# Optimization experiments

Hardware: AMD Instinct MI355X
Metric: run time of the kernel (lower is better)

Reference implementation:

```python
import jax, jax.numpy as jnp
import numpy as np

B, N, L, D, IN, H = 16, 100, 90, 300, 256, 256


def setup_inputs() -> dict:
    key = jax.random.key(0)
    ks = jax.random.split(key, 24)
    s = 0.02
    inp = {}
    inp["h_local"] = jax.random.normal(ks[0], (B, N, IN), jnp.float32)
    inp["items_review"] = jax.random.normal(ks[1], (B, N, L, D), jnp.float32)
    inp["adj_sg"] = jax.random.randint(ks[2], (B, N, 2 * N), 0, 2, jnp.int32)
    inp["attn_review_mask"] = jnp.zeros((B, N, L), jnp.bool_)
    # BatchNorm affine params (eval mode, running_mean=0, running_var=1)
    inp["bn_gamma"] = jnp.ones((IN,), jnp.float32)
    inp["bn_beta"] = jnp.zeros((IN,), jnp.float32)
    # MultiHeadAttention linear layers (review_dim=300)
    inp["W_q"] = jax.random.normal(ks[3], (D, D), jnp.float32) * s
    inp["b_q"] = jnp.zeros((D,), jnp.float32)
    inp["W_k"] = jax.random.normal(ks[4], (D, D), jnp.float32) * s
    inp["b_k"] = jnp.zeros((D,), jnp.float32)
    inp["W_v"] = jax.random.normal(ks[5], (D, D), jnp.float32) * s
    inp["b_v"] = jnp.zeros((D,), jnp.float32)
    inp["W_f"] = jax.random.normal(ks[6], (D, D), jnp.float32) * s
    inp["b_f"] = jnp.zeros((D,), jnp.float32)
    # fc: input_size -> hidden_size
    inp["W_fc"] = jax.random.normal(ks[7], (H, IN), jnp.float32) * s
    inp["b_fc"] = jnp.zeros((H,), jnp.float32)
    # edge linear layers
    inp["W_in"] = jax.random.normal(ks[8], (H, H), jnp.float32) * s
    inp["b_in"] = jnp.zeros((H,), jnp.float32)
    inp["W_out"] = jax.random.normal(ks[9], (H, H), jnp.float32) * s
    inp["b_out"] = jnp.zeros((H,), jnp.float32)
    inp["b_iah"] = jax.random.normal(ks[10], (H,), jnp.float32) * s
    inp["b_oah"] = jax.random.normal(ks[11], (H,), jnp.float32) * s
    # fc_in_out: 2H -> H
    inp["W_io"] = jax.random.normal(ks[12], (H, 2 * H), jnp.float32) * s
    inp["b_io"] = jnp.zeros((H,), jnp.float32)
    return inp


def reference(h_local, items_review, adj_sg, attn_review_mask,
              bn_gamma, bn_beta,
              W_q, b_q, W_k, b_k, W_v, b_v, W_f, b_f,
              W_fc, b_fc, W_in, b_in, W_out, b_out,
              b_iah, b_oah, W_io, b_io):
    n = h_local.shape[1]
    # BatchNorm1d (eval mode: running_mean=0, running_var=1) + fc
    h = h_local * (bn_gamma / jnp.sqrt(1.0 + 1e-5)) + bn_beta
    hidden = h @ W_fc.T + b_fc                                  # [B,N,H]

    # MultiHeadAttention over reviews (heads never split in original bmm)
    q = items_review @ W_q.T + b_q                              # [B,N,L,D]
    k = items_review @ W_k.T + b_k
    v = items_review @ W_v.T + b_v
    scale = (items_review.shape[-1] // 3) ** (-0.5)             # (300//3)^-0.5 = 0.1
    attn = jax.nn.softmax(jnp.einsum('bnld,bnmd->bnlm', q, k) * scale, axis=-1)
    ctx = jnp.einsum('bnlm,bnmd->bnld', attn, v)
    out_attn = items_review + (ctx @ W_f.T + b_f)               # residual
    h_review = jnp.sum(out_attn, axis=2)                        # [B,N,D] sum over review_len

    # pairwise cosine similarity (torch.cosine_similarity, eps=1e-8)
    norms = jnp.linalg.norm(h_review, axis=-1)                  # [B,N]
    sim = jnp.einsum('bnd,bmd->bnm', h_review, h_review) \
        / jnp.maximum(norms[:, :, None] * norms[:, None, :], 1e-8)

    adj_in = adj_sg[:, :, :n] > 0
    adj_out = adj_sg[:, :, n:2 * n] > 0
    NEG = jnp.float32(-9e15)
    sim_in = jax.nn.softmax(jnp.where(adj_in, sim, NEG), axis=-1)
    sim_out = jax.nn.softmax(jnp.where(adj_out, sim, NEG), axis=-1)

    input_in = jnp.einsum('bnm,bmh->bnh', sim_in, hidden @ W_in.T + b_in) + b_iah
    input_out = jnp.einsum('bnm,bmh->bnh', sim_out, hidden @ W_out.T + b_out) + b_oah
    output = jnp.concatenate([input_in, input_out], axis=-1) @ W_io.T + b_io
    return output
```

## Files before the change

### kernel.cpp

```cpp
#include <hip/hip_runtime.h>
#include <math.h>

#define Bb 16
#define Nn 100
#define Ll 90
#define Dd 300
#define NBLK (Bb*Nn)
#define LP 96
#define DP 320
#define DPH 40

typedef __attribute__((ext_vector_type(8))) short short8v;
typedef __attribute__((ext_vector_type(4))) short short4v;
typedef __attribute__((ext_vector_type(4))) float f32x4;

__device__ __forceinline__ unsigned short f2bf(float f) {
  unsigned int u = __float_as_uint(f);
  u += 0x7fffu + ((u >> 16) & 1u);
  return (unsigned short)(u >> 16);
}
__device__ __forceinline__ float bf2f(unsigned short h) {
  return __uint_as_float(((unsigned int)h) << 16);
}

__global__ __launch_bounds__(256) void k_matM(const float* __restrict__ Wq,
                                              const float* __restrict__ Wk,
                                              unsigned short* __restrict__ Mb) {
  int idx = blockIdx.x * 256 + threadIdx.x;
  if (idx >= DP * DP) return;
  int i = idx / DP, j = idx % DP;
  float s = 0.f;
  if (i < Dd && j < Dd) {
    for (int o = 0; o < Dd; o++) s += Wq[o * Dd + i] * Wk[o * Dd + j];
  }
  Mb[idx] = f2bf(s);
}

__global__ __launch_bounds__(256) void k_matG(const float* __restrict__ Wf,
                                              const float* __restrict__ Wv,
                                              float* __restrict__ G) {
  int idx = blockIdx.x * 256 + threadIdx.x;
  if (idx >= Dd * 304) return;
  int o = idx / 304, p = idx % 304;
  float s = 0.f;
  if (p < Dd) {
    for (int v = 0; v < Dd; v++) s += Wf[o * Dd + v] * Wv[v * Dd + p];
  }
  G[idx] = s;
}

__global__ void k_vec(const float* __restrict__ Wq, const float* __restrict__ Wk,
                      const float* __restrict__ Wf,
                      const float* __restrict__ bq, const float* __restrict__ bk,
                      const float* __restrict__ bv, const float* __restrict__ bf,
                      float* __restrict__ uv, float* __restrict__ tv,
                      float* __restrict__ cv, float* __restrict__ bias2) {
  int t = threadIdx.x;
  if (t < 304) {
    float su = 0.f, st = 0.f, sb = 0.f;
    if (t < Dd) {
      for (int o = 0; o < Dd; o++) {
        su += Wq[o * Dd + t] * bk[o];
        st += Wk[o * Dd + t] * bq[o];
      }
      for (int v = 0; v < Dd; v++) sb += Wf[t * Dd + v] * bv[v];
      sb = 90.f * (sb + bf[t]);
    }
    uv[t] = su; tv[t] = st; bias2[t] = sb;
  }
  if (t == 511) {
    float s = 0.f;
    for (int o = 0; o < Dd; o++) s += bq[o] * bk[o];
    cv[0] = s;
  }
}

__global__ __launch_bounds__(256) void k_mm256(
    const float* __restrict__ A0, const float* __restrict__ A1, int lda,
    const float* __restrict__ B0, const float* __restrict__ B1, int ldb,
    float* __restrict__ C, int ldc, const float* __restrict__ gamma) {
  const float* A = blockIdx.z ? A1 : A0;
  const float* B = blockIdx.z ? B1 : B0;
  float* Cb = C + (size_t)blockIdx.z * 256 * ldc;
  __shared__ float As[16][68];
  __shared__ float Bs[16][68];
  int m0 = blockIdx.x * 64, n0 = blockIdx.y * 64;
  int tx = threadIdx.x & 15, ty = threadIdx.x >> 4;
  float acc[4][4];
#pragma unroll
  for (int i = 0; i < 4; i++)
#pragma unroll
    for (int j = 0; j < 4; j++) acc[i][j] = 0.f;
  int r = threadIdx.x >> 2;
  int kq = (threadIdx.x & 3) << 2;
  int kk2 = threadIdx.x >> 4;
  int nq = (threadIdx.x & 15) << 2;
  for (int k0 = 0; k0 < 256; k0 += 16) {
    {
      float4 v = *(const float4*)(A + (size_t)(m0 + r) * lda + k0 + kq);
      As[kq + 0][r] = v.x; As[kq + 1][r] = v.y; As[kq + 2][r] = v.z; As[kq + 3][r] = v.w;
    }
    {
      float4 v = *(const float4*)(B + (size_t)(k0 + kk2) * ldb + n0 + nq);
      Bs[kk2][nq + 0] = v.x; Bs[kk2][nq + 1] = v.y; Bs[kk2][nq + 2] = v.z; Bs[kk2][nq + 3] = v.w;
    }
    __syncthreads();
#pragma unroll
    for (int kk = 0; kk < 16; kk++) {
      float4 av = *(const float4*)&As[kk][ty * 4];
      float4 bv = *(const float4*)&Bs[kk][tx * 4];
      acc[0][0] += av.x * bv.x; acc[0][1] += av.x * bv.y; acc[0][2] += av.x * bv.z; acc[0][3] += av.x * bv.w;
      acc[1][0] += av.y * bv.x; acc[1][1] += av.y * bv.y; acc[1][2] += av.y * bv.z; acc[1][3] += av.y * bv.w;
      acc[2][0] += av.z * bv.x; acc[2][1] += av.z * bv.y; acc[2][2] += av.z * bv.z; acc[2][3] += av.z * bv.w;
      acc[3][0] += av.w * bv.x; acc[3][1] += av.w * bv.y; acc[3][2] += av.w * bv.z; acc[3][3] += av.w * bv.w;
    }
    __syncthreads();
  }
  const float bninv = rsqrtf(1.00001f);
#pragma unroll
  for (int i = 0; i < 4; i++) {
    int gm = m0 + ty * 4 + i;
#pragma unroll
    for (int j = 0; j < 4; j++) {
      int gn = n0 + tx * 4 + j;
      float v = acc[i][j];
      if (gamma) v *= gamma[gn] * bninv;
      Cb[(size_t)gm * ldc + gn] = v;
    }
  }
}

__global__ __launch_bounds__(256) void k_vecd(
    const float* __restrict__ W_fc, const float* __restrict__ b_fc,
    const float* __restrict__ beta,
    const float* __restrict__ W_in, const float* __restrict__ b_in,
    const float* __restrict__ b_iah,
    const float* __restrict__ W_out, const float* __restrict__ b_out,
    const float* __restrict__ b_oah,
    const float* __restrict__ W_io, const float* __restrict__ b_io,
    float* __restrict__ dvec) {
  __shared__ float v1[256];
  __shared__ float v23[512];
  int i = threadIdx.x;
  float s = 0.f;
  for (int k = 0; k < 256; k++) s += W_fc[i * 256 + k] * beta[k];
  v1[i] = s + b_fc[i];
  __syncthreads();
  float s2 = 0.f, s3 = 0.f;
  for (int k = 0; k < 256; k++) {
    float vk = v1[k];
    s2 += W_in[i * 256 + k] * vk;
    s3 += W_out[i * 256 + k] * vk;
  }
  v23[i] = s2 + b_in[i] + b_iah[i];
  v23[256 + i] = s3 + b_out[i] + b_oah[i];
  __syncthreads();
  float sd = 0.f;
  for (int k = 0; k < 512; k++) sd += W_io[i * 512 + k] * v23[k];
  dvec[i] = sd + b_io[i];
}

__global__ __launch_bounds__(512, 4) void k_attn(
    const float* __restrict__ items, const unsigned short* __restrict__ Mb,
    const float* __restrict__ uvec, const float* __restrict__ tvec,
    const float* __restrict__ cval_p,
    float* __restrict__ r_all, float* __restrict__ colsum_all) {
  __shared__ unsigned short Xs[LP * DP];
  __shared__ unsigned short Zc[LP * 64];
  __shared__ float ulv[LP], tmv[LP], wsum[LP];
  __shared__ float ulds[304], tlds[304];

  const int tid = threadIdx.x;
  const int bid = blockIdx.x;
  const float* Xg = items + (size_t)bid * (Ll * Dd);
  const float cval = cval_p[0];

  for (int c = tid; c < LP * DPH; c += 512) {
    int l = c / DPH, ch = c % DPH, d0 = ch * 8;
    float v[8];
    if (l < Ll && d0 < Dd) {
      if (d0 + 8 <= Dd) {
        float4 a = *(const float4*)(Xg + l * Dd + d0);
        float4 b = *(const float4*)(Xg + l * Dd + d0 + 4);
        v[0] = a.x; v[1] = a.y; v[2] = a.z; v[3] = a.w;
        v[4] = b.x; v[5] = b.y; v[6] = b.z; v[7] = b.w;
      } else {
#pragma unroll
        for (int q = 0; q < 8; q++) { int d = d0 + q; v[q] = (d < Dd) ? Xg[l * Dd + d] : 0.f; }
      }
    } else {
#pragma unroll
      for (int q = 0; q < 8; q++) v[q] = 0.f;
    }
    short8v pk;
#pragma unroll
    for (int q = 0; q < 8; q++) pk[q] = (short)f2bf(v[q]);
    *(short8v*)((char*)Xs + l * 640 + ((d0 * 2) ^ ((l & 7) << 4))) = pk;
  }
  for (int d = tid; d < 304; d += 512) { ulds[d] = uvec[d]; tlds[d] = tvec[d]; }
  if (tid < LP) wsum[tid] = 0.f;
  for (int d = tid; d < 304; d += 512) {
    float s = 0.f;
    if (d < Dd) {
      for (int l = 0; l < Ll; l++) s += Xg[l * Dd + d];
    }
    colsum_all[(size_t)bid * 304 + d] = s;
  }
  __syncthreads();

  if (tid < 384) {
    int row = tid >> 2, q = tid & 3;
    float su = 0.f, st = 0.f;
    if (row < Ll) {
      for (int ii = 0; ii < 75; ii++) {
        int i = q * 75 + ii;
        float xv = bf2f(Xs[(row * 640 + ((i * 2) ^ ((row & 7) << 4))) >> 1]);
        su += xv * ulds[i];
        st += xv * tlds[i];
      }
    }
    su += __shfl_xor(su, 1); su += __shfl_xor(su, 2);
    st += __shfl_xor(st, 1); st += __shfl_xor(st, 2);
    if (q == 0) { ulv[row] = su; tmv[row] = st; }
  }
  __syncthreads();

  const int lane = tid & 63, wave = tid >> 6;
  const int fr = lane & 15, kg = lane >> 4;

  f32x4 acc[6];
#pragma unroll
  for (int mt = 0; mt < 6; mt++) acc[mt] = (f32x4){0.f, 0.f, 0.f, 0.f};

  for (int c = 0; c < 5; c++) {
    for (int t = wave; t < 24; t += 8) {
      int ict = t / 6, mt = t % 6;
      int irow = c * 64 + ict * 16 + fr;
      f32x4 zacc = (f32x4){0.f, 0.f, 0.f, 0.f};
#pragma unroll
      for (int ks = 0; ks < 10; ks++) {
        short8v a = *(const short8v*)(Mb + irow * DP + ks * 32 + kg * 8);
        int brow = mt * 16 + fr;
        short8v b = *(const short8v*)((char*)Xs + brow * 640 +
                                      (((ks * 32 + kg * 8) * 2) ^ ((brow & 7) << 4)));
        zacc = __builtin_amdgcn_mfma_f32_16x16x32_bf16(a, b, zacc, 0, 0, 0);
      }
      int m = mt * 16 + fr;
      int ic0 = ict * 16 + kg * 4;
      short4v pk;
#pragma unroll
      for (int r2 = 0; r2 < 4; r2++) pk[r2] = (short)f2bf(zacc[r2]);
      *(short4v*)((char*)Zc + m * 128 + ((ic0 * 2) ^ ((m & 7) << 4))) = pk;
    }
    __syncthreads();
    if (wave < 6) {
#pragma unroll
      for (int mt = 0; mt < 6; mt++) {
#pragma unroll
        for (int ks = 0; ks < 2; ks++) {
          int arow = wave * 16 + fr;
          short8v a = *(const short8v*)((char*)Xs + arow * 640 +
                                        (((c * 64 + ks * 32 + kg * 8) * 2) ^ ((arow & 7) << 4)));
          int brow = mt * 16 + fr;
          short8v b = *(const short8v*)((char*)Zc + brow * 128 +
                                        (((ks * 32 + kg * 8) * 2) ^ ((brow & 7) << 4)));
          acc[mt] = __builtin_amdgcn_mfma_f32_16x16x32_bf16(a, b, acc[mt], 0, 0, 0);
        }
      }
    }
    __syncthreads();
  }

  if (wave < 6) {
    float tmc[6];
#pragma unroll
    for (int mt = 0; mt < 6; mt++) tmc[mt] = tmv[mt * 16 + fr];
    float colpart[6] = {0.f, 0.f, 0.f, 0.f, 0.f, 0.f};
#pragma unroll
    for (int r2 = 0; r2 < 4; r2++) {
      int l = wave * 16 + kg * 4 + r2;
      float base = ulv[l] + cval;
      float x[6];
#pragma unroll
      for (int mt = 0; mt < 6; mt++) {
        int col = mt * 16 + fr;
        x[mt] = (col < Ll) ? 0.1f * (acc[mt][r2] + base + tmc[mt]) : -INFINITY;
      }
      float mx = x[0];
#pragma unroll
      for (int mt = 1; mt < 6; mt++) mx = fmaxf(mx, x[mt]);
      mx = fmaxf(mx, __shfl_xor(mx, 1));
      mx = fmaxf(mx, __shfl_xor(mx, 2));
      mx = fmaxf(mx, __shfl_xor(mx, 4));
      mx = fmaxf(mx, __shfl_xor(mx, 8));
      float e[6]; float s = 0.f;
#pragma unroll
      for (int mt = 0; mt < 6; mt++) { e[mt] = __expf(x[mt] - mx); s += e[mt]; }
      s += __shfl_xor(s, 1); s += __shfl_xor(s, 2);
      s += __shfl_xor(s, 4); s += __shfl_xor(s, 8);
      float inv = 1.f / s;
      if (l < Ll) {
#pragma unroll
        for (int mt = 0; mt < 6; mt++) colpart[mt] += e[mt] * inv;
      }
    }
#pragma unroll
    for (int mt = 0; mt < 6; mt++) {
      colpart[mt] += __shfl_xor(colpart[mt], 16);
      colpart[mt] += __shfl_xor(colpart[mt], 32);
    }
    if (lane < 16) {
#pragma unroll
      for (int mt = 0; mt < 6; mt++) atomicAdd(&wsum[mt * 16 + fr], colpart[mt]);
    }
  }
  __syncthreads();

  for (int i = tid; i < 304; i += 512) {
    float s = 0.f;
    if (i < Dd) {
      for (int m = 0; m < Ll; m++)
        s += wsum[m] * bf2f(Xs[(m * 640 + ((i * 2) ^ ((m & 7) << 4))) >> 1]);
    }
    r_all[(size_t)bid * 304 + i] = s;
  }
}

__global__ __launch_bounds__(256) void k_gemm_bt(
    const float* __restrict__ A, int lda, const float* __restrict__ W, int ldw,
    const float* __restrict__ bias, const float* __restrict__ res, int ldres,
    float* __restrict__ C, int ldc, int Mdim, int Ndim, int Kdim) {
  __shared__ float As[16][68];
  __shared__ float Bs[16][68];
  int m0 = blockIdx.x * 64, n0 = blockIdx.y * 64;
  int tx = threadIdx.x & 15, ty = threadIdx.x >> 4;
  float acc[4][4];
#pragma unroll
  for (int i = 0; i < 4; i++)
#pragma unroll
    for (int j = 0; j < 4; j++) acc[i][j] = 0.f;
  int r = threadIdx.x >> 2;
  int kq = (threadIdx.x & 3) << 2;
  for (int k0 = 0; k0 < Kdim; k0 += 16) {
    {
      int gm = m0 + r;
      float4 v = {0.f, 0.f, 0.f, 0.f};
      if (gm < Mdim) v = *(const float4*)(A + (size_t)gm * lda + k0 + kq);
      As[kq + 0][r] = v.x; As[kq + 1][r] = v.y; As[kq + 2][r] = v.z; As[kq + 3][r] = v.w;
    }
    {
      int gn = n0 + r;
      float4 v = {0.f, 0.f, 0.f, 0.f};
      if (gn < Ndim) v = *(const float4*)(W + (size_t)gn * ldw + k0 + kq);
      Bs[kq + 0][r] = v.x; Bs[kq + 1][r] = v.y; Bs[kq + 2][r] = v.z; Bs[kq + 3][r] = v.w;
    }
    __syncthreads();
#pragma unroll
    for (int kk = 0; kk < 16; kk++) {
      float4 av = *(const float4*)&As[kk][ty * 4];
      float4 bv = *(const float4*)&Bs[kk][tx * 4];
      acc[0][0] += av.x * bv.x; acc[0][1] += av.x * bv.y; acc[0][2] += av.x * bv.z; acc[0][3] += av.x * bv.w;
      acc[1][0] += av.y * bv.x; acc[1][1] += av.y * bv.y; acc[1][2] += av.y * bv.z; acc[1][3] += av.y * bv.w;
      acc[2][0] += av.z * bv.x; acc[2][1] += av.z * bv.y; acc[2][2] += av.z * bv.z; acc[2][3] += av.z * bv.w;
      acc[3][0] += av.w * bv.x; acc[3][1] += av.w * bv.y; acc[3][2] += av.w * bv.z; acc[3][3] += av.w * bv.w;
    }
    __syncthreads();
  }
#pragma unroll
  for (int i = 0; i < 4; i++) {
    int gm = m0 + ty * 4 + i;
    if (gm >= Mdim) continue;
#pragma unroll
    for (int j = 0; j < 4; j++) {
      int gn = n0 + tx * 4 + j;
      if (gn >= Ndim) continue;
      float v = acc[i][j];
      if (bias) v += bias[gn];
      if (res) v += res[(size_t)gm * ldres + gn];
      C[(size_t)gm * ldc + gn] = v;
    }
  }
}

__global__ __launch_bounds__(256) void k_norm(const float* __restrict__ hrev,
                                              unsigned short* __restrict__ Hn) {
  int row = blockIdx.x * 4 + (threadIdx.x >> 6);
  int lane = threadIdx.x & 63;
  float v[5]; float ss = 0.f;
#pragma unroll
  for (int j = 0; j < 5; j++) {
    int i = lane + j * 64;
    float x = (i < Dd) ? hrev[(size_t)row * 304 + i] : 0.f;
    v[j] = x; ss += x * x;
  }
#pragma unroll
  for (int o = 32; o; o >>= 1) ss += __shfl_xor(ss, o);
  float inv = (ss > 0.f) ? rsqrtf(ss) : 0.f;
#pragma unroll
  for (int j = 0; j < 5; j++) {
    int i = lane + j * 64;
    if (i < DP) Hn[(size_t)row * DP + i] = f2bf(v[j] * inv);
  }
}

__global__ __launch_bounds__(512) void k_simgram(
    const unsigned short* __restrict__ Hn, const int* __restrict__ adj,
    float* __restrict__ simin, float* __restrict__ simout) {
  __shared__ unsigned short HL[112 * DP];
  int b = blockIdx.x, tid = threadIdx.x;
  for (int c = tid; c < 112 * DPH; c += 512) {
    int rb = c / DPH, ch = c % DPH;
    short8v v;
    if (rb < Nn) v = *(const short8v*)(Hn + ((size_t)(b * Nn + rb)) * DP + ch * 8);
    else {
#pragma unroll
      for (int q = 0; q < 8; q++) v[q] = 0;
    }
    *(short8v*)((char*)HL + rb * 640 + ((ch * 16) ^ ((rb & 7) << 4))) = v;
  }
  __syncthreads();
  const int lane = tid & 63, wave = tid >> 6;
  const int fr = lane & 15, kg = lane >> 4;
  if (wave < 7) {
    f32x4 acc[7];
#pragma unroll
    for (int mt = 0; mt < 7; mt++) acc[mt] = (f32x4){0.f, 0.f, 0.f, 0.f};
#pragma unroll
    for (int mt = 0; mt < 7; mt++) {
#pragma unroll
      for (int ks = 0; ks < 10; ks++) {
        int ar = wave * 16 + fr;
        short8v a = *(const short8v*)((char*)HL + ar * 640 +
                                      (((ks * 32 + kg * 8) * 2) ^ ((ar & 7) << 4)));
        int br = mt * 16 + fr;
        short8v bb = *(const short8v*)((char*)HL + br * 640 +
                                       (((ks * 32 + kg * 8) * 2) ^ ((br & 7) << 4)));
        acc[mt] = __builtin_amdgcn_mfma_f32_16x16x32_bf16(a, bb, acc[mt], 0, 0, 0);
      }
    }
    const int* adjb = adj + (size_t)b * Nn * 2 * Nn;
#pragma unroll
    for (int which = 0; which < 2; which++) {
      float* dst = which ? simout : simin;
#pragma unroll
      for (int r2 = 0; r2 < 4; r2++) {
        int l = wave * 16 + kg * 4 + r2;
        bool lv = l < Nn;
        float x[7];
#pragma unroll
        for (int mt = 0; mt < 7; mt++) {
          int col = mt * 16 + fr;
          bool cvd = col < Nn;
          int am = (lv && cvd) ? adjb[l * (2 * Nn) + which * Nn + col] : 0;
          x[mt] = cvd ? ((am > 0) ? acc[mt][r2] : -9e15f) : -INFINITY;
        }
        float mx = x[0];
#pragma unroll
        for (int mt = 1; mt < 7; mt++) mx = fmaxf(mx, x[mt]);
        mx = fmaxf(mx, __shfl_xor(mx, 1));
        mx = fmaxf(mx, __shfl_xor(mx, 2));
        mx = fmaxf(mx, __shfl_xor(mx, 4));
        mx = fmaxf(mx, __shfl_xor(mx, 8));
        float e[7]; float s = 0.f;
#pragma unroll
        for (int mt = 0; mt < 7; mt++) { e[mt] = __expf(x[mt] - mx); s += e[mt]; }
        s += __shfl_xor(s, 1); s += __shfl_xor(s, 2);
        s += __shfl_xor(s, 4); s += __shfl_xor(s, 8);
        float inv = 1.f / s;
        if (lv) {
#pragma unroll
          for (int mt = 0; mt < 7; mt++) {
            int col = mt * 16 + fr;
            if (col < Nn) dst[((size_t)(b * Nn + l)) * Nn + col] = e[mt] * inv;
          }
        }
      }
    }
  }
}

__global__ __launch_bounds__(256) void k_mixout(
    const float* __restrict__ simin, const float* __restrict__ simout,
    const float* __restrict__ P, const float* __restrict__ dvec,
    float* __restrict__ out) {
  __shared__ float si[Nn], so[Nn];
  int bn = blockIdx.x, h = threadIdx.x, b = bn / Nn;
  if (h < Nn) {
    si[h] = simin[(size_t)bn * Nn + h];
    so[h] = simout[(size_t)bn * Nn + h];
  }
  __syncthreads();
  const float* Pb = P + (size_t)b * Nn * 512;
  float acc = dvec[h];
  for (int m = 0; m < Nn; m++)
    acc += si[m] * Pb[m * 512 + h] + so[m] * Pb[m * 512 + 256 + h];
  out[(size_t)bn * 256 + h] = acc;
}

extern "C" void kernel_launch(void* const* d_in, const int* in_sizes, int n_in,
                              void* d_out, int out_size, void* d_ws, size_t ws_size,
                              hipStream_t stream) {
  (void)in_sizes; (void)n_in; (void)out_size; (void)ws_size;
  const float* h_local = (const float*)d_in[0];
  const float* items   = (const float*)d_in[1];
  const int*   adj     = (const int*)d_in[2];
  const float* bn_g  = (const float*)d_in[4];
  const float* bn_b  = (const float*)d_in[5];
  const float* W_q = (const float*)d_in[6];   const float* b_q = (const float*)d_in[7];
  const float* W_k = (const float*)d_in[8];   const float* b_k = (const float*)d_in[9];
  const float* W_v = (const float*)d_in[10];  const float* b_v = (const float*)d_in[11];
  const float* W_f = (const float*)d_in[12];  const float* b_f = (const float*)d_in[13];
  const float* W_fc = (const float*)d_in[14]; const float* b_fc = (const float*)d_in[15];
  const float* W_in = (const float*)d_in[16]; const float* b_in = (const float*)d_in[17];
  const float* W_out = (const float*)d_in[18]; const float* b_out = (const float*)d_in[19];
  const float* b_iah = (const float*)d_in[20]; const float* b_oah = (const float*)d_in[21];
  const float* W_io = (const float*)d_in[22];  const float* b_io = (const float*)d_in[23];
  float* out = (float*)d_out;

  char* w = (char*)d_ws;
  auto alloc = [&](size_t bytes) { char* p = w; w += (bytes + 255) & ~(size_t)255; return p; };
  unsigned short* Mb = (unsigned short*)alloc((size_t)DP * DP * 2);
  float* G      = (float*)alloc((size_t)Dd * 304 * 4);
  float* uv     = (float*)alloc(304 * 4);
  float* tv     = (float*)alloc(304 * 4);
  float* cv     = (float*)alloc(256);
  float* bias2  = (float*)alloc(304 * 4);
  float* Tbuf   = (float*)alloc((size_t)512 * 256 * 4);
  float* Bcat   = (float*)alloc((size_t)512 * 256 * 4);
  float* dvec   = (float*)alloc(256 * 4);
  float* r_all  = (float*)alloc((size_t)NBLK * 304 * 4);
  float* colsum = (float*)alloc((size_t)NBLK * 304 * 4);
  float* hrev   = (float*)alloc((size_t)NBLK * 304 * 4);
  unsigned short* Hn = (unsigned short*)alloc((size_t)NBLK * DP * 2);
  float* simin  = (float*)alloc((size_t)NBLK * Nn * 4);
  float* simout = (float*)alloc((size_t)NBLK * Nn * 4);
  float* P      = (float*)alloc((size_t)NBLK * 512 * 4);

  k_matM<<<(DP * DP + 255) / 256, 256, 0, stream>>>(W_q, W_k, Mb);
  k_matG<<<(Dd * 304 + 255) / 256, 256, 0, stream>>>(W_f, W_v, G);
  k_vec<<<1, 512, 0, stream>>>(W_q, W_k, W_f, b_q, b_k, b_v, b_f, uv, tv, cv, bias2);
  {
    dim3 g(4, 4, 2);
    k_mm256<<<g, 256, 0, stream>>>(W_in, W_out, 256, W_fc, W_fc, 256, Tbuf, 256, nullptr);
    k_mm256<<<g, 256, 0, stream>>>(W_io, W_io + 256, 512, Tbuf, Tbuf + 256 * 256, 256,
                                   Bcat, 256, bn_g);
  }
  k_vecd<<<1, 256, 0, stream>>>(W_fc, b_fc, bn_b, W_in, b_in, b_iah,
                                W_out, b_out, b_oah, W_io, b_io, dvec);

  {
    dim3 g(25, 8);
    k_gemm_bt<<<g, 256, 0, stream>>>(h_local, 256, Bcat, 256, nullptr, nullptr, 0,
                                     P, 512, NBLK, 512, 256);
  }

  k_attn<<<NBLK, 512, 0, stream>>>(items, Mb, uv, tv, cv, r_all, colsum);
  {
    dim3 g(25, 5);
    k_gemm_bt<<<g, 256, 0, stream>>>(r_all, 304, G, 304, bias2, colsum, 304,
                                     hrev, 304, NBLK, 300, 304);
  }
  k_norm<<<NBLK / 4, 256, 0, stream>>>(hrev, Hn);
  k_simgram<<<Bb, 512, 0, stream>>>(Hn, adj, simin, simout);
  k_mixout<<<NBLK, 256, 0, stream>>>(simin, simout, P, dvec, out);
}
```

Before: 775.8 us.

## Fold Q/K biases into augmented bilinear matrix and merge setup kernels

Adds a ones column at index 300 of the bf16 item tile and an extra row/column of the M matrix holding the bq/bk terms, so the bias corrections come out of the MFMA directly. That removes the per-row u/t dot products, their shared buffers and the k_vec kernel. The three weight-precompute kernels become one k_setup launch. The attention inner loop is restructured to keep three independent MFMA accumulators per wave with precomputed addresses. k_simgram is split into 7 single-wave blocks per batch that read from global memory, and several loops get unroll pragmas. The bias terms now go through bf16 rounding inside the MFMA, which may shift accuracy slightly.

```diff
diff --git a/kernel.cpp b/kernel.cpp
--- a/kernel.cpp
+++ b/kernel.cpp
@@ -23,55 +23,48 @@
   return __uint_as_float(((unsigned int)h) << 16);
 }
 
-__global__ __launch_bounds__(256) void k_matM(const float* __restrict__ Wq,
-                                              const float* __restrict__ Wk,
-                                              unsigned short* __restrict__ Mb) {
-  int idx = blockIdx.x * 256 + threadIdx.x;
-  if (idx >= DP * DP) return;
-  int i = idx / DP, j = idx % DP;
-  float s = 0.f;
-  if (i < Dd && j < Dd) {
-    for (int o = 0; o < Dd; o++) s += Wq[o * Dd + i] * Wk[o * Dd + j];
-  }
-  Mb[idx] = f2bf(s);
-}
-
-__global__ __launch_bounds__(256) void k_matG(const float* __restrict__ Wf,
-                                              const float* __restrict__ Wv,
-                                              float* __restrict__ G) {
-  int idx = blockIdx.x * 256 + threadIdx.x;
-  if (idx >= Dd * 304) return;
-  int o = idx / 304, p = idx % 304;
-  float s = 0.f;
-  if (p < Dd) {
-    for (int v = 0; v < Dd; v++) s += Wf[o * Dd + v] * Wv[v * Dd + p];
-  }
-  G[idx] = s;
-}
-
-__global__ void k_vec(const float* __restrict__ Wq, const float* __restrict__ Wk,
-                      const float* __restrict__ Wf,
-                      const float* __restrict__ bq, const float* __restrict__ bk,
-                      const float* __restrict__ bv, const float* __restrict__ bf,
-                      float* __restrict__ uv, float* __restrict__ tv,
-                      float* __restrict__ cv, float* __restrict__ bias2) {
-  int t = threadIdx.x;
-  if (t < 304) {
-    float su = 0.f, st = 0.f, sb = 0.f;
-    if (t < Dd) {
+__global__ __launch_bounds__(256) void k_setup(
+    const float* __restrict__ Wq, const float* __restrict__ Wk,
+    const float* __restrict__ bq, const float* __restrict__ bk,
+    const float* __restrict__ Wf, const float* __restrict__ Wv,
+    const float* __restrict__ bv, const float* __restrict__ bf,
+    unsigned short* __restrict__ Mb, float* __restrict__ G,
+    float* __restrict__ bias2) {
+  int blk = blockIdx.x;
+  if (blk < 400) {
+    int idx = blk * 256 + threadIdx.x;
+    int i = idx / DP, j = idx % DP;
+    float s = 0.f;
+    if (i <= Dd && j <= Dd) {
+#pragma unroll 10
       for (int o = 0; o < Dd; o++) {
-        su += Wq[o * Dd + t] * bk[o];
-        st += Wk[o * Dd + t] * bq[o];
-      }
-      for (int v = 0; v < Dd; v++) sb += Wf[t * Dd + v] * bv[v];
-      sb = 90.f * (sb + bf[t]);
-    }
-    uv[t] = su; tv[t] = st; bias2[t] = sb;
-  }
-  if (t == 511) {
-    float s = 0.f;
-    for (int o = 0; o < Dd; o++) s += bq[o] * bk[o];
-    cv[0] = s;
+        float av = (i < Dd) ? Wq[o * Dd + i] : bq[o];
+        float bw = (j < Dd) ? Wk[o * Dd + j] : bk[o];
+        s += av * bw;
+      }
+    }
+    Mb[idx] = f2bf(s);
+  } else if (blk < 757) {
+    int idx = (blk - 400) * 256 + threadIdx.x;
+    if (idx < Dd * 304) {
+      int o = idx / 304, p = idx % 304;
+      float s = 0.f;
+      if (p < Dd) {
+#pragma unroll 10
+        for (int v = 0; v < Dd; v++) s += Wf[o * Dd + v] * Wv[v * Dd + p];
+      }
+      G[idx] = s;
+    }
+  } else {
+    for (int t = threadIdx.x; t < 304; t += 256) {
+      float sb = 0.f;
+      if (t < Dd) {
+#pragma unroll 10
+        for (int v = 0; v < Dd; v++) sb += Wf[t * Dd + v] * bv[v];
+        sb = 90.f * (sb + bf[t]);
+      }
+      bias2[t] = sb;
+    }
   }
 }
 
@@ -143,10 +136,12 @@
   __shared__ float v23[512];
   int i = threadIdx.x;
   float s = 0.f;
+#pragma unroll 16
   for (int k = 0; k < 256; k++) s += W_fc[i * 256 + k] * beta[k];
   v1[i] = s + b_fc[i];
   __syncthreads();
   float s2 = 0.f, s3 = 0.f;
+#pragma unroll 16
   for (int k = 0; k < 256; k++) {
     float vk = v1[k];
     s2 += W_in[i * 256 + k] * vk;
@@ -156,24 +151,23 @@
   v23[256 + i] = s3 + b_out[i] + b_oah[i];
   __syncthreads();
   float sd = 0.f;
+#pragma unroll 16
   for (int k = 0; k < 512; k++) sd += W_io[i * 512 + k] * v23[k];
   dvec[i] = sd + b_io[i];
 }
 
 __global__ __launch_bounds__(512, 4) void k_attn(
     const float* __restrict__ items, const unsigned short* __restrict__ Mb,
-    const float* __restrict__ uvec, const float* __restrict__ tvec,
-    const float* __restrict__ cval_p,
     float* __restrict__ r_all, float* __restrict__ colsum_all) {
   __shared__ unsigned short Xs[LP * DP];
   __shared__ unsigned short Zc[LP * 64];
-  __shared__ float ulv[LP], tmv[LP], wsum[LP];
-  __shared__ float ulds[304], tlds[304];
+  __shared__ float wsum[LP];
 
   const int tid = threadIdx.x;
   const int bid = blockIdx.x;
   const float* Xg = items + (size_t)bid * (Ll * Dd);
-  const float cval = cval_p[0];
+
+  if (tid < LP) wsum[tid] = 0.f;
 
   for (int c = tid; c < LP * DPH; c += 512) {
     int l = c / DPH, ch = c % DPH, d0 = ch * 8;
@@ -186,7 +180,10 @@
         v[4] = b.x; v[5] = b.y; v[6] = b.z; v[7] = b.w;
       } else {
 #pragma unroll
-        for (int q = 0; q < 8; q++) { int d = d0 + q; v[q] = (d < Dd) ? Xg[l * Dd + d] : 0.f; }
+        for (int q = 0; q < 8; q++) {
+          int d = d0 + q;
+          v[q] = (d < Dd) ? Xg[l * Dd + d] : ((d == Dd) ? 1.f : 0.f);
+        }
       }
     } else {
 #pragma unroll
@@ -197,71 +194,73 @@
     for (int q = 0; q < 8; q++) pk[q] = (short)f2bf(v[q]);
     *(short8v*)((char*)Xs + l * 640 + ((d0 * 2) ^ ((l & 7) << 4))) = pk;
   }
-  for (int d = tid; d < 304; d += 512) { ulds[d] = uvec[d]; tlds[d] = tvec[d]; }
-  if (tid < LP) wsum[tid] = 0.f;
+
   for (int d = tid; d < 304; d += 512) {
     float s = 0.f;
     if (d < Dd) {
+#pragma unroll 18
       for (int l = 0; l < Ll; l++) s += Xg[l * Dd + d];
     }
     colsum_all[(size_t)bid * 304 + d] = s;
-  }
-  __syncthreads();
-
-  if (tid < 384) {
-    int row = tid >> 2, q = tid & 3;
-    float su = 0.f, st = 0.f;
-    if (row < Ll) {
-      for (int ii = 0; ii < 75; ii++) {
-        int i = q * 75 + ii;
-        float xv = bf2f(Xs[(row * 640 + ((i * 2) ^ ((row & 7) << 4))) >> 1]);
-        su += xv * ulds[i];
-        st += xv * tlds[i];
-      }
-    }
-    su += __shfl_xor(su, 1); su += __shfl_xor(su, 2);
-    st += __shfl_xor(st, 1); st += __shfl_xor(st, 2);
-    if (q == 0) { ulv[row] = su; tmv[row] = st; }
   }
   __syncthreads();
 
   const int lane = tid & 63, wave = tid >> 6;
   const int fr = lane & 15, kg = lane >> 4;
 
+  int itile[3], bbyte[3], bswz[3], mrow[3], icol0[3];
+#pragma unroll
+  for (int tt = 0; tt < 3; tt++) {
+    int t = wave + tt * 8;
+    int ict = t / 6, mt = t - ict * 6;
+    itile[tt] = ict * 16 + fr;
+    int brow = mt * 16 + fr;
+    bbyte[tt] = brow * 640;
+    bswz[tt] = (brow & 7) << 4;
+    mrow[tt] = brow;
+    icol0[tt] = ict * 16 + kg * 4;
+  }
+
   f32x4 acc[6];
 #pragma unroll
   for (int mt = 0; mt < 6; mt++) acc[mt] = (f32x4){0.f, 0.f, 0.f, 0.f};
 
   for (int c = 0; c < 5; c++) {
-    for (int t = wave; t < 24; t += 8) {
-      int ict = t / 6, mt = t % 6;
-      int irow = c * 64 + ict * 16 + fr;
-      f32x4 zacc = (f32x4){0.f, 0.f, 0.f, 0.f};
-#pragma unroll
-      for (int ks = 0; ks < 10; ks++) {
-        short8v a = *(const short8v*)(Mb + irow * DP + ks * 32 + kg * 8);
-        int brow = mt * 16 + fr;
-        short8v b = *(const short8v*)((char*)Xs + brow * 640 +
-                                      (((ks * 32 + kg * 8) * 2) ^ ((brow & 7) << 4)));
-        zacc = __builtin_amdgcn_mfma_f32_16x16x32_bf16(a, b, zacc, 0, 0, 0);
-      }
-      int m = mt * 16 + fr;
-      int ic0 = ict * 16 + kg * 4;
+    f32x4 z0 = (f32x4){0.f, 0.f, 0.f, 0.f}, z1 = z0, z2 = z0;
+    const unsigned short* MbC = Mb + (size_t)(c * 64) * DP;
+#pragma unroll
+    for (int ks = 0; ks < 10; ks++) {
+      int koff = ks * 32 + kg * 8;
+      short8v a0 = *(const short8v*)(MbC + itile[0] * DP + koff);
+      short8v b0 = *(const short8v*)((char*)Xs + bbyte[0] + ((koff * 2) ^ bswz[0]));
+      z0 = __builtin_amdgcn_mfma_f32_16x16x32_bf16(a0, b0, z0, 0, 0, 0);
+      short8v a1 = *(const short8v*)(MbC + itile[1] * DP + koff);
+      short8v b1 = *(const short8v*)((char*)Xs + bbyte[1] + ((koff * 2) ^ bswz[1]));
+      z1 = __builtin_amdgcn_mfma_f32_16x16x32_bf16(a1, b1, z1, 0, 0, 0);
+      short8v a2 = *(const short8v*)(MbC + itile[2] * DP + koff);
+      short8v b2 = *(const short8v*)((char*)Xs + bbyte[2] + ((koff * 2) ^ bswz[2]));
+      z2 = __builtin_amdgcn_mfma_f32_16x16x32_bf16(a2, b2, z2, 0, 0, 0);
+    }
+#pragma unroll
+    for (int tt = 0; tt < 3; tt++) {
+      f32x4 z = tt == 0 ? z0 : (tt == 1 ? z1 : z2);
       short4v pk;
 #pragma unroll
-      for (int r2 = 0; r2 < 4; r2++) pk[r2] = (short)f2bf(zacc[r2]);
-      *(short4v*)((char*)Zc + m * 128 + ((ic0 * 2) ^ ((m & 7) << 4))) = pk;
+      for (int r2 = 0; r2 < 4; r2++) pk[r2] = (short)f2bf(z[r2]);
+      *(short4v*)((char*)Zc + mrow[tt] * 128 +
+                  ((icol0[tt] * 2) ^ ((mrow[tt] & 7) << 4))) = pk;
     }
     __syncthreads();
     if (wave < 6) {
+      int arow = wave * 16 + fr;
+      int abyte = arow * 640, aswz = (arow & 7) << 4;
 #pragma unroll
       for (int mt = 0; mt < 6; mt++) {
+        int brow = mt * 16 + fr;
 #pragma unroll
         for (int ks = 0; ks < 2; ks++) {
-          int arow = wave * 16 + fr;
-          short8v a = *(const short8v*)((char*)Xs + arow * 640 +
-                                        (((c * 64 + ks * 32 + kg * 8) * 2) ^ ((arow & 7) << 4)));
-          int brow = mt * 16 + fr;
+          short8v a = *(const short8v*)((char*)Xs + abyte +
+                                        (((c * 64 + ks * 32 + kg * 8) * 2) ^ aswz));
           short8v b = *(const short8v*)((char*)Zc + brow * 128 +
                                         (((ks * 32 + kg * 8) * 2) ^ ((brow & 7) << 4)));
           acc[mt] = __builtin_amdgcn_mfma_f32_16x16x32_bf16(a, b, acc[mt], 0, 0, 0);
@@ -272,19 +271,15 @@
   }
 
   if (wave < 6) {
-    float tmc[6];
-#pragma unroll
-    for (int mt = 0; mt < 6; mt++) tmc[mt] = tmv[mt * 16 + fr];
     float colpart[6] = {0.f, 0.f, 0.f, 0.f, 0.f, 0.f};
 #pragma unroll
     for (int r2 = 0; r2 < 4; r2++) {
       int l = wave * 16 + kg * 4 + r2;
-      float base = ulv[l] + cval;
       float x[6];
 #pragma unroll
       for (int mt = 0; mt < 6; mt++) {
         int col = mt * 16 + fr;
-        x[mt] = (col < Ll) ? 0.1f * (acc[mt][r2] + base + tmc[mt]) : -INFINITY;
+        x[mt] = (col < Ll) ? 0.1f * acc[mt][r2] : -INFINITY;
       }
       float mx = x[0];
 #pragma unroll
@@ -319,6 +314,7 @@
   for (int i = tid; i < 304; i += 512) {
     float s = 0.f;
     if (i < Dd) {
+#pragma unroll 15
       for (int m = 0; m < Ll; m++)
         s += wsum[m] * bf2f(Xs[(m * 640 + ((i * 2) ^ ((m & 7) << 4))) >> 1]);
     }
@@ -403,76 +399,65 @@
   }
 }
 
-__global__ __launch_bounds__(512) void k_simgram(
+__global__ __launch_bounds__(64) void k_simgram(
     const unsigned short* __restrict__ Hn, const int* __restrict__ adj,
     float* __restrict__ simin, float* __restrict__ simout) {
-  __shared__ unsigned short HL[112 * DP];
-  int b = blockIdx.x, tid = threadIdx.x;
-  for (int c = tid; c < 112 * DPH; c += 512) {
-    int rb = c / DPH, ch = c % DPH;
-    short8v v;
-    if (rb < Nn) v = *(const short8v*)(Hn + ((size_t)(b * Nn + rb)) * DP + ch * 8);
-    else {
-#pragma unroll
-      for (int q = 0; q < 8; q++) v[q] = 0;
-    }
-    *(short8v*)((char*)HL + rb * 640 + ((ch * 16) ^ ((rb & 7) << 4))) = v;
-  }
-  __syncthreads();
-  const int lane = tid & 63, wave = tid >> 6;
-  const int fr = lane & 15, kg = lane >> 4;
-  if (wave < 7) {
-    f32x4 acc[7];
-#pragma unroll
-    for (int mt = 0; mt < 7; mt++) acc[mt] = (f32x4){0.f, 0.f, 0.f, 0.f};
+  int b = blockIdx.x, rt = blockIdx.y;
+  int lane = threadIdx.x;
+  int fr = lane & 15, kg = lane >> 4;
+  const unsigned short* Hb = Hn + (size_t)b * Nn * DP;
+  int ar = rt * 16 + fr;
+  short8v zerov;
+#pragma unroll
+  for (int q = 0; q < 8; q++) zerov[q] = 0;
+  f32x4 acc[7];
+#pragma unroll
+  for (int mt = 0; mt < 7; mt++) acc[mt] = (f32x4){0.f, 0.f, 0.f, 0.f};
+#pragma unroll
+  for (int ks = 0; ks < 10; ks++) {
+    int koff = ks * 32 + kg * 8;
+    short8v a = (ar < Nn) ? *(const short8v*)(Hb + (size_t)ar * DP + koff) : zerov;
 #pragma unroll
     for (int mt = 0; mt < 7; mt++) {
-#pragma unroll
-      for (int ks = 0; ks < 10; ks++) {
-        int ar = wave * 16 + fr;
-        short8v a = *(const short8v*)((char*)HL + ar * 640 +
-                                      (((ks * 32 + kg * 8) * 2) ^ ((ar & 7) << 4)));
-        int br = mt * 16 + fr;
-        short8v bb = *(const short8v*)((char*)HL + br * 640 +
-                                       (((ks * 32 + kg * 8) * 2) ^ ((br & 7) << 4)));
-        acc[mt] = __builtin_amdgcn_mfma_f32_16x16x32_bf16(a, bb, acc[mt], 0, 0, 0);
-      }
-    }
-    const int* adjb = adj + (size_t)b * Nn * 2 * Nn;
-#pragma unroll
-    for (int which = 0; which < 2; which++) {
-      float* dst = which ? simout : simin;
-#pragma unroll
-      for (int r2 = 0; r2 < 4; r2++) {
-        int l = wave * 16 + kg * 4 + r2;
-        bool lv = l < Nn;
-        float x[7];
+      int br = mt * 16 + fr;
+      short8v bb = (br < Nn) ? *(const short8v*)(Hb + (size_t)br * DP + koff) : zerov;
+      acc[mt] = __builtin_amdgcn_mfma_f32_16x16x32_bf16(a, bb, acc[mt], 0, 0, 0);
+    }
+  }
+  const int* adjb = adj + (size_t)b * Nn * 2 * Nn;
+#pragma unroll
+  for (int which = 0; which < 2; which++) {
+    float* dst = which ? simout : simin;
+#pragma unroll
+    for (int r2 = 0; r2 < 4; r2++) {
+      int l = rt * 16 + kg * 4 + r2;
+      bool lv = l < Nn;
+      float x[7];
+#pragma unroll
+      for (int mt = 0; mt < 7; mt++) {
+        int col = mt * 16 + fr;
+        bool cvd = col < Nn;
+        int am = (lv && cvd) ? adjb[l * (2 * Nn) + which * Nn + col] : 0;
+        x[mt] = cvd ? ((am > 0) ? acc[mt][r2] : -9e15f) : -INFINITY;
+      }
+      float mx = x[0];
+#pragma unroll
+      for (int mt = 1; mt < 7; mt++) mx = fmaxf(mx, x[mt]);
+      mx = fmaxf(mx, __shfl_xor(mx, 1));
+      mx = fmaxf(mx, __shfl_xor(mx, 2));
+      mx = fmaxf(mx, __shfl_xor(mx, 4));
+      mx = fmaxf(mx, __shfl_xor(mx, 8));
+      float e[7]; float s = 0.f;
+#pragma unroll
+      for (int mt = 0; mt < 7; mt++) { e[mt] = __expf(x[mt] - mx); s += e[mt]; }
+      s += __shfl_xor(s, 1); s += __shfl_xor(s, 2);
+      s += __shfl_xor(s, 4); s += __shfl_xor(s, 8);
+      float inv = 1.f / s;
+      if (lv) {
 #pragma unroll
         for (int mt = 0; mt < 7; mt++) {
           int col = mt * 16 + fr;
-          bool cvd = col < Nn;
-          int am = (lv && cvd) ? adjb[l * (2 * Nn) + which * Nn + col] : 0;
-          x[mt] = cvd ? ((am > 0) ? acc[mt][r2] : -9e15f) : -INFINITY;
-        }
-        float mx = x[0];
-#pragma unroll
-        for (int mt = 1; mt < 7; mt++) mx = fmaxf(mx, x[mt]);
-        mx = fmaxf(mx, __shfl_xor(mx, 1));
-        mx = fmaxf(mx, __shfl_xor(mx, 2));
-        mx = fmaxf(mx, __shfl_xor(mx, 4));
-        mx = fmaxf(mx, __shfl_xor(mx, 8));
-        float e[7]; float s = 0.f;
-#pragma unroll
-        for (int mt = 0; mt < 7; mt++) { e[mt] = __expf(x[mt] - mx); s += e[mt]; }
-        s += __shfl_xor(s, 1); s += __shfl_xor(s, 2);
-        s += __shfl_xor(s, 4); s += __shfl_xor(s, 8);
-        float inv = 1.f / s;
-        if (lv) {
-#pragma unroll
-          for (int mt = 0; mt < 7; mt++) {
-            int col = mt * 16 + fr;
-            if (col < Nn) dst[((size_t)(b * Nn + l)) * Nn + col] = e[mt] * inv;
-          }
+          if (col < Nn) dst[((size_t)(b * Nn + l)) * Nn + col] = e[mt] * inv;
         }
       }
     }
@@ -492,6 +477,7 @@
   __syncthreads();
   const float* Pb = P + (size_t)b * Nn * 512;
   float acc = dvec[h];
+#pragma unroll 10
   for (int m = 0; m < Nn; m++)
     acc += si[m] * Pb[m * 512 + h] + so[m] * Pb[m * 512 + 256 + h];
   out[(size_t)bn * 256 + h] = acc;
@@ -521,9 +507,6 @@
   auto alloc = [&](size_t bytes) { char* p = w; w += (bytes + 255) & ~(size_t)255; return p; };
   unsigned short* Mb = (unsigned short*)alloc((size_t)DP * DP * 2);
   float* G      = (float*)alloc((size_t)Dd * 304 * 4);
-  float* uv     = (float*)alloc(304 * 4);
-  float* tv     = (float*)alloc(304 * 4);
-  float* cv     = (float*)alloc(256);
   float* bias2  = (float*)alloc(304 * 4);
   float* Tbuf   = (float*)alloc((size_t)512 * 256 * 4);
   float* Bcat   = (float*)alloc((size_t)512 * 256 * 4);
@@ -536,9 +519,10 @@
   float* simout = (float*)alloc((size_t)NBLK * Nn * 4);
   float* P      = (float*)alloc((size_t)NBLK * 512 * 4);
 
-  k_matM<<<(DP * DP + 255) / 256, 256, 0, stream>>>(W_q, W_k, Mb);
-  k_matG<<<(Dd * 304 + 255) / 256, 256, 0, stream>>>(W_f, W_v, G);
-  k_vec<<<1, 512, 0, stream>>>(W_q, W_k, W_f, b_q, b_k, b_v, b_f, uv, tv, cv, bias2);
+  k_setup<<<758, 256, 0, stream>>>(W_q, W_k, b_q, b_k, W_f, W_v, b_v, b_f,
+                                   Mb, G, bias2);
+  k_attn<<<NBLK, 512, 0, stream>>>(items, Mb, r_all, colsum);
+
   {
     dim3 g(4, 4, 2);
     k_mm256<<<g, 256, 0, stream>>>(W_in, W_out, 256, W_fc, W_fc, 256, Tbuf, 256, nullptr);
@@ -547,20 +531,20 @@
   }
   k_vecd<<<1, 256, 0, stream>>>(W_fc, b_fc, bn_b, W_in, b_in, b_iah,
                                 W_out, b_out, b_oah, W_io, b_io, dvec);
-
   {
     dim3 g(25, 8);
     k_gemm_bt<<<g, 256, 0, stream>>>(h_local, 256, Bcat, 256, nullptr, nullptr, 0,
                                      P, 512, NBLK, 512, 256);
   }
-
-  k_attn<<<NBLK, 512, 0, stream>>>(items, Mb, uv, tv, cv, r_all, colsum);
   {
     dim3 g(25, 5);
     k_gemm_bt<<<g, 256, 0, stream>>>(r_all, 304, G, 304, bias2, colsum, 304,
                                      hrev, 304, NBLK, 300, 304);
   }
   k_norm<<<NBLK / 4, 256, 0, stream>>>(hrev, Hn);
-  k_simgram<<<Bb, 512, 0, stream>>>(Hn, adj, simin, simout);
+  {
+    dim3 g(Bb, 7);
+    k_simgram<<<g, 64, 0, stream>>>(Hn, adj, simin, simout);
+  }
   k_mixout<<<NBLK, 256, 0, stream>>>(simin, simout, P, dvec, out);
 }
```

Result: faster. 747.2 us (-3.7%).
